# Kernel optimization log

Measured on AMD Instinct MI355X. Metric: run time of the kernel, lower is better.

The kernel has to match this reference:

```python
import jax, jax.numpy as jnp
import numpy as np

H = 56; W = 56; WS = 7; SHIFT = 3; C = 256; NH = 8
HD = C // NH; N = WS * WS; NW = (H // WS) * (W // WS)
SCALE = HD ** -0.5
LN_EPS = 1e-5


def _rel_pos_index():
    coords = np.stack(np.meshgrid(np.arange(WS), np.arange(WS), indexing='ij'))  # (2, ws, ws)
    cf = coords.reshape(2, -1)
    rel = (cf[:, :, None] - cf[:, None, :]).transpose(1, 2, 0)  # (N, N, 2)
    rel[..., 0] += WS - 1
    rel[..., 1] += WS - 1
    rel[..., 0] *= 2 * WS - 1
    return rel.sum(-1)  # (N, N) indices into (2*ws-1)^2 table

RPI = jnp.asarray(_rel_pos_index())


def _attn_mask():
    img = np.zeros((H, W))
    slices = (slice(0, -WS), slice(-WS, -SHIFT), slice(-SHIFT, None))
    cnt = 0
    for hs in slices:
        for ws_ in slices:
            img[hs, ws_] = cnt
            cnt += 1
    mw = img.reshape(H // WS, WS, W // WS, WS).transpose(0, 2, 1, 3).reshape(-1, N)
    diff = mw[:, None, :] - mw[:, :, None]  # (nW, N, N), [w,i,j] = mw[w,j]-mw[w,i]
    return jnp.asarray(np.where(diff != 0, -100.0, 0.0).astype(np.float32))

AMASK = _attn_mask()  # (nW, N, N)


def ln(x, g, b):
    m = x.mean(-1, keepdims=True)
    v = x.var(-1, keepdims=True)
    return (x - m) / jnp.sqrt(v + LN_EPS) * g + b


def win_part(x):  # (B, H, W, C) -> (B*nW, N, C)
    B = x.shape[0]
    return x.reshape(B, H // WS, WS, W // WS, WS, C).transpose(0, 1, 3, 2, 4, 5).reshape(-1, N, C)


def win_rev(xw, B):  # (B*nW, N, C) -> (B, H, W, C)
    return xw.reshape(B, H // WS, W // WS, WS, WS, C).transpose(0, 1, 3, 2, 4, 5).reshape(B, H, W, C)


def setup_inputs() -> dict:
    key = jax.random.key(0)
    ks = iter(jax.random.split(key, 40))
    B, L = 16, H * W
    Ch = int(C * 4.0)
    p = {}
    p['x'] = jax.random.normal(next(ks), (B, L, C), jnp.float32)
    p['x_SAR'] = jax.random.normal(next(ks), (B, L, C), jnp.float32)
    p['ln1_g'] = jnp.ones((C,)); p['ln1_b'] = jnp.zeros((C,))
    p['ln1s_g'] = jnp.ones((C,)); p['ln1s_b'] = jnp.zeros((C,))
    p['qkv_w'] = jax.random.normal(next(ks), (3 * C, C)) * 0.02
    p['qkv_b'] = jnp.zeros((3 * C,))
    p['qkvs_w'] = jax.random.normal(next(ks), (3 * C, C)) * 0.02
    p['qkvs_b'] = jnp.zeros((3 * C,))
    p['rpb_table'] = jax.random.normal(next(ks), ((2 * WS - 1) ** 2, NH)) * 0.02
    p['fuse_w'] = jax.random.normal(next(ks), (NH, NH)) * 0.1  # Conv2d(8,8,1) weight squeezed
    p['fuse_b'] = jnp.zeros((NH,))
    p['proj_w'] = jax.random.normal(next(ks), (C, C)) * 0.02
    p['proj_b'] = jnp.zeros((C,))
    p['projs_w'] = jax.random.normal(next(ks), (C, C)) * 0.02
    p['projs_b'] = jnp.zeros((C,))
    p['ln2_g'] = jnp.ones((C,)); p['ln2_b'] = jnp.zeros((C,))
    p['ln2s_g'] = jnp.ones((C,)); p['ln2s_b'] = jnp.zeros((C,))
    p['fc1_w'] = jax.random.normal(next(ks), (Ch, C)) * 0.02
    p['fc1_b'] = jnp.zeros((Ch,))
    p['fc2_w'] = jax.random.normal(next(ks), (C, Ch)) * 0.02
    p['fc2_b'] = jnp.zeros((C,))
    p['fc1s_w'] = jax.random.normal(next(ks), (Ch, C)) * 0.02
    p['fc1s_b'] = jnp.zeros((Ch,))
    p['fc2s_w'] = jax.random.normal(next(ks), (C, Ch)) * 0.02
    p['fc2s_b'] = jnp.zeros((C,))
    return p


def reference(x, x_SAR, ln1_g, ln1_b, ln1s_g, ln1s_b, qkv_w, qkv_b, qkvs_w, qkvs_b,
              rpb_table, fuse_w, fuse_b, proj_w, proj_b, projs_w, projs_b,
              ln2_g, ln2_b, ln2s_g, ln2s_b, fc1_w, fc1_b, fc2_w, fc2_b,
              fc1s_w, fc1s_b, fc2s_w, fc2s_b):
    B = x.shape[0]
    sc, sc_s = x, x_SAR

    def pre(xx, g, b):  # norm -> spatial -> cyclic shift -> windows
        xs = ln(xx, g, b).reshape(B, H, W, C)
        xs = jnp.roll(xs, (-SHIFT, -SHIFT), axis=(1, 2))
        return win_part(xs)

    xw = pre(x, ln1_g, ln1_b)
    xws = pre(x_SAR, ln1s_g, ln1s_b)

    def qkv_f(xin, Wt, bt):
        qkv = (xin @ Wt.T + bt).reshape(-1, N, 3, NH, HD).transpose(2, 0, 3, 1, 4)
        return qkv[0], qkv[1], qkv[2]  # each (B*nW, nH, N, HD)

    q, k, v = qkv_f(xw, qkv_w, qkv_b)
    qs, ks_, vs = qkv_f(xws, qkvs_w, qkvs_b)

    attn = jnp.einsum('bhnd,bhmd->bhnm', q * SCALE, k)
    attn_s = jnp.einsum('bhnd,bhmd->bhnm', qs * SCALE, ks_)

    rpb = rpb_table[RPI.reshape(-1)].reshape(N, N, NH).transpose(2, 0, 1)  # (nH, N, N)
    attn = attn + rpb[None]
    attn_s = attn_s + rpb[None]

    # shift-window mask add
    attn = (attn.reshape(B, NW, NH, N, N) + AMASK[None, :, None]).reshape(-1, NH, N, N)
    attn_s = (attn_s.reshape(B, NW, NH, N, N) + AMASK[None, :, None]).reshape(-1, NH, N, N)

    # dual-branch fusion: 1x1 conv over head dim + sigmoid gate
    diff = attn_s - attn
    gate = jax.nn.sigmoid(jnp.einsum('oh,bhnm->bonm', fuse_w, diff) + fuse_b[None, :, None, None])
    attn_f = jax.nn.softmax(attn + diff * gate, axis=-1)
    attn_s = jax.nn.softmax(attn_s, axis=-1)

    def out_f(a, vv, pw, pb):
        o = jnp.einsum('bhnm,bhmd->bhnd', a, vv).transpose(0, 2, 1, 3).reshape(-1, N, C)
        return o @ pw.T + pb

    xo = out_f(attn_f, v, proj_w, proj_b)
    xos = out_f(attn_s, vs, projs_w, projs_b)

    def post(xout, scc, g2, b2, w1, b1, w2, b2m):
        xr = jnp.roll(win_rev(xout, B), (SHIFT, SHIFT), axis=(1, 2)).reshape(B, -1, C)
        xr = scc + xr
        h = jax.nn.gelu(ln(xr, g2, b2) @ w1.T + b1, approximate=False)
        return xr + (h @ w2.T + b2m)

    out = post(xo, sc, ln2_g, ln2_b, fc1_w, fc1_b, fc2_w, fc2_b)
    out_s = post(xos, sc_s, ln2s_g, ln2s_b, fc1s_w, fc1s_b, fc2s_w, fc2s_b)
    return out, out_s
```

## Files before the change

### kernel.cpp

```cpp
#include <hip/hip_runtime.h>
#include <hip/hip_bf16.h>
#include <cstdio>

typedef unsigned short ushort_t;
using bf16x8  = __attribute__((ext_vector_type(8))) __bf16;
using u16x8   = __attribute__((ext_vector_type(8))) unsigned short;
using floatx4 = __attribute__((ext_vector_type(4))) float;

constexpr int    kTokens = 50176;
constexpr size_t TCsz    = (size_t)kTokens * 256;
constexpr float  kScale  = 0.17677669529663687f;
constexpr int    SPITCH  = 56;
constexpr size_t VTP     = 2048;
constexpr size_t VTSZ    = (size_t)8192 * VTP;

__device__ __forceinline__ float bf2f(ushort_t u) {
  unsigned int x = (unsigned int)u << 16;
  return __uint_as_float(x);
}
__device__ __forceinline__ ushort_t f2bf(float f) {
  __hip_bfloat16 h = __float2bfloat16(f);
  return *(ushort_t*)&h;
}

__device__ __forceinline__ void gl_lds16(const ushort_t* g, ushort_t* l) {
  __builtin_amdgcn_global_load_lds(
      (const __attribute__((address_space(1))) unsigned int*)g,
      (__attribute__((address_space(3))) unsigned int*)l, 16, 0, 0);
}

__global__ __launch_bounds__(256) void f2b_k(const float* __restrict__ src,
                                             ushort_t* __restrict__ dst, int n) {
  int i = blockIdx.x * 256 + threadIdx.x;
  if (i < n) dst[i] = f2bf(src[i]);
}

__global__ __launch_bounds__(64) void bias2_k(const float* __restrict__ rpb,
                                              float* __restrict__ biasf) {
  const int b = blockIdx.x;
  const int head = b & 7, chunk = (b >> 3) & 3, cls = b >> 5;
  const int wh7 = cls >> 1, ww7 = cls & 1;
  const int lane = threadIdx.x;
  float* bp = biasf + ((size_t)b * 64 + lane) * 16;
#pragma unroll
  for (int nt = 0; nt < 4; ++nt) {
#pragma unroll
    for (int r = 0; r < 4; ++r) {
      const int row = chunk * 16 + (lane >> 4) * 4 + r;
      const int col = nt * 16 + (lane & 15);
      float val = 0.0f;
      if (row < 49 && col < 49) {
        const int yi = row / 7, xi = row % 7, yj = col / 7, xj = col % 7;
        val = rpb[((yi - yj + 6) * 13 + (xi - xj + 6)) * 8 + head];
        const int li = (wh7 ? (yi < 4 ? 1 : 2) : 0) * 3 + (ww7 ? (xi < 4 ? 1 : 2) : 0);
        const int lj = (wh7 ? (yj < 4 ? 1 : 2) : 0) * 3 + (ww7 ? (xj < 4 ? 1 : 2) : 0);
        if (li != lj) val -= 100.0f;
      }
      bp[nt * 4 + r] = val;
    }
  }
}

__global__ __launch_bounds__(256) void vtz_k(ushort_t* __restrict__ vtA,
                                             ushort_t* __restrict__ vtB) {
  const int id = blockIdx.x * 256 + threadIdx.x;
  ushort_t* base = (id < 262144) ? vtA : vtB;
  const size_t r = (size_t)(id & 262143) * 64;
  const uint4 z{0, 0, 0, 0};
  *(uint4*)(base + r + 48) = z;
  *(uint4*)(base + r + 56) = z;
}

template <int SHIFTED>
__global__ __launch_bounds__(256) void ln_k(const float* __restrict__ x,
                                            const float* __restrict__ g,
                                            const float* __restrict__ b,
                                            ushort_t* __restrict__ yout) {
  const int wave = threadIdx.x >> 6, lane = threadIdx.x & 63;
  const int t = blockIdx.x * 4 + wave;
  size_t src;
  if (SHIFTED) {
    int bb = t / 3136, r = t % 3136;
    int wi = r / 49, n = r % 49;
    int hp = (wi >> 3) * 7 + n / 7;
    int wp = (wi & 7) * 7 + n % 7;
    int sh = hp + 3; if (sh >= 56) sh -= 56;
    int sw = wp + 3; if (sw >= 56) sw -= 56;
    src = ((size_t)bb * 3136 + sh * 56 + sw) * 256;
  } else {
    src = (size_t)t * 256;
  }
  const float4 v4 = *(const float4*)(x + src + lane * 4);
  float s  = v4.x + v4.y + v4.z + v4.w;
  float s2 = v4.x * v4.x + v4.y * v4.y + v4.z * v4.z + v4.w * v4.w;
#pragma unroll
  for (int off = 32; off > 0; off >>= 1) {
    s  += __shfl_xor(s,  off);
    s2 += __shfl_xor(s2, off);
  }
  const float mean = s * (1.0f / 256.0f);
  const float var  = s2 * (1.0f / 256.0f) - mean * mean;
  const float rstd = rsqrtf(var + 1e-5f);
  const float4 g4 = *(const float4*)(g + lane * 4);
  const float4 b4 = *(const float4*)(b + lane * 4);
  ushort4 o;
  o.x = f2bf((v4.x - mean) * rstd * g4.x + b4.x);
  o.y = f2bf((v4.y - mean) * rstd * g4.y + b4.y);
  o.z = f2bf((v4.z - mean) * rstd * g4.z + b4.z);
  o.w = f2bf((v4.w - mean) * rstd * g4.w + b4.w);
  *(ushort4*)(yout + (size_t)t * 256 + lane * 4) = o;
}

template <int MODE>
__global__ __launch_bounds__(256) void bgemm_k(const ushort_t* __restrict__ A,
                                               const ushort_t* __restrict__ W,
                                               const float* __restrict__ bias,
                                               float* __restrict__ outf,
                                               ushort_t* __restrict__ outb,
                                               const float* __restrict__ aux,
                                               int K, int Nc) {
  __shared__ __align__(16) ushort_t As[128 * 32];
  __shared__ __align__(16) ushort_t Bs[128 * 32];
  const int tid = threadIdx.x;
  const int nbx = gridDim.x;
  const int nwg = nbx * gridDim.y;
  int flat = blockIdx.y * nbx + blockIdx.x;
  {
    const int xcd = flat & 7, idx = flat >> 3;
    const int q8 = nwg >> 3, r8 = nwg & 7;
    flat = (xcd < r8 ? xcd * (q8 + 1) : r8 * (q8 + 1) + (xcd - r8) * q8) + idx;
  }
  const int m0 = (flat / nbx) * 128;
  const int n0 = (flat % nbx) * 128;
  const int lane = tid & 63, wv = tid >> 6;
  const int wm = (wv >> 1) * 64, wn = (wv & 1) * 64;
  const int l16 = lane & 15, quad = lane >> 4;

  const int srow = tid >> 2;
  const int gkc  = (tid & 3) ^ ((tid >> 3) & 3);
  const ushort_t* Ag0 = A + (size_t)(m0 + srow) * K + gkc * 8;
  const ushort_t* Ag1 = A + (size_t)(m0 + 64 + srow) * K + gkc * 8;
  const ushort_t* Wg0 = W + (size_t)(n0 + srow) * K + gkc * 8;
  const ushort_t* Wg1 = W + (size_t)(n0 + 64 + srow) * K + gkc * 8;
  ushort_t* AsW0 = As + wv * 512;
  ushort_t* AsW1 = As + 2048 + wv * 512;
  ushort_t* BsW0 = Bs + wv * 512;
  ushort_t* BsW1 = Bs + 2048 + wv * 512;

  const int kcq = quad ^ ((l16 >> 1) & 3);
  const int arA = (wm + l16) * 32 + kcq * 8;
  const int arB = (wn + l16) * 32 + kcq * 8;

  floatx4 acc[4][4] = {};
  for (int k0 = 0; k0 < K; k0 += 32) {
    gl_lds16(Ag0, AsW0);
    gl_lds16(Ag1, AsW1);
    gl_lds16(Wg0, BsW0);
    gl_lds16(Wg1, BsW1);
    Ag0 += 32; Ag1 += 32; Wg0 += 32; Wg1 += 32;
    __syncthreads();
    bf16x8 af[4], bfr[4];
#pragma unroll
    for (int t = 0; t < 4; ++t) {
      af[t]  = *(const bf16x8*)&As[arA + t * 512];
      bfr[t] = *(const bf16x8*)&Bs[arB + t * 512];
    }
#pragma unroll
    for (int mt = 0; mt < 4; ++mt)
#pragma unroll
      for (int nt = 0; nt < 4; ++nt)
        acc[mt][nt] = __builtin_amdgcn_mfma_f32_16x16x32_bf16(af[mt], bfr[nt], acc[mt][nt], 0, 0, 0);
    __syncthreads();
  }

  if (MODE == 0) {
    int wis[16], ns[16];
#pragma unroll
    for (int mt = 0; mt < 4; ++mt) {
      int row = m0 + wm + mt * 16 + quad * 4;
      int wi = row / 49, n = row - wi * 49;
#pragma unroll
      for (int r = 0; r < 4; ++r) {
        wis[mt * 4 + r] = wi; ns[mt * 4 + r] = n;
        if (++n == 49) { n = 0; ++wi; }
      }
    }
    if (n0 < 512) {
      size_t rb[16];
#pragma unroll
      for (int i = 0; i < 16; ++i) rb[i] = (size_t)wis[i] * 12544 + (size_t)ns[i] * 32;
#pragma unroll
      for (int nt = 0; nt < 4; ++nt) {
        const int col = n0 + wn + nt * 16 + l16;
        const int which = col >> 8, head = (col >> 5) & 7, d = col & 31;
        const float bv = bias[col];
        const float sc = (which == 0) ? kScale : 1.0f;
        ushort_t* ob = outb + (size_t)which * TCsz + head * 1568 + d;
#pragma unroll
        for (int i = 0; i < 16; ++i)
          ob[rb[i]] = f2bf((acc[i >> 2][nt][i & 3] + bv) * sc);
      }
    } else {
      size_t rb[16];
#pragma unroll
      for (int i = 0; i < 16; ++i) rb[i] = (size_t)wis[i] * 16384 + (size_t)ns[i];
      ushort_t* vtb = (ushort_t*)outf;
#pragma unroll
      for (int nt = 0; nt < 4; ++nt) {
        const int col = n0 + wn + nt * 16 + l16;
        const int head = (col >> 5) & 7, d = col & 31;
        const float bv = bias[col];
        ushort_t* ob = vtb + head * 2048 + d * 64;
#pragma unroll
        for (int i = 0; i < 16; ++i)
          ob[rb[i]] = f2bf(acc[i >> 2][nt][i & 3] + bv);
      }
    }
  } else if (MODE == 1) {
    size_t rb[16];
#pragma unroll
    for (int mt = 0; mt < 4; ++mt) {
#pragma unroll
      for (int r = 0; r < 4; ++r) {
        const int row = m0 + wm + mt * 16 + quad * 4 + r;
        const int wi = row / 49, n = row - wi * 49;
        const int b = wi >> 6, wl = wi & 63;
        int h = (wl >> 3) * 7 + n / 7 + 3; if (h >= 56) h -= 56;
        int w = (wl & 7) * 7 + n % 7 + 3; if (w >= 56) w -= 56;
        rb[mt * 4 + r] = ((size_t)(b * 3136 + h * 56 + w)) * 256;
      }
    }
#pragma unroll
    for (int nt = 0; nt < 4; ++nt) {
      const int col = n0 + wn + nt * 16 + l16;
      const float bv = bias[col];
#pragma unroll
      for (int i = 0; i < 16; ++i) {
        const size_t idx = rb[i] + col;
        outf[idx] = aux[idx] + acc[i >> 2][nt][i & 3] + bv;
      }
    }
  } else if (MODE == 2) {
    size_t rb[16];
#pragma unroll
    for (int mt = 0; mt < 4; ++mt)
#pragma unroll
      for (int r = 0; r < 4; ++r)
        rb[mt * 4 + r] = (size_t)(m0 + wm + mt * 16 + quad * 4 + r) * Nc;
#pragma unroll
    for (int nt = 0; nt < 4; ++nt) {
      const int col = n0 + wn + nt * 16 + l16;
      const float bv = bias[col];
#pragma unroll
      for (int i = 0; i < 16; ++i) {
        float val = acc[i >> 2][nt][i & 3] + bv;
        val = 0.5f * val * (1.0f + erff(val * 0.70710678118654752f));
        outb[rb[i] + col] = f2bf(val);
      }
    }
  } else {
    size_t rb[16];
#pragma unroll
    for (int mt = 0; mt < 4; ++mt)
#pragma unroll
      for (int r = 0; r < 4; ++r)
        rb[mt * 4 + r] = (size_t)(m0 + wm + mt * 16 + quad * 4 + r) * 256;
#pragma unroll
    for (int nt = 0; nt < 4; ++nt) {
      const int col = n0 + wn + nt * 16 + l16;
      const float bv = bias[col];
#pragma unroll
      for (int i = 0; i < 16; ++i) {
        const size_t idx = rb[i] + col;
        outf[idx] = aux[idx] + acc[i >> 2][nt][i & 3] + bv;
      }
    }
  }
}

__global__ __launch_bounds__(256) void attn_k(const ushort_t* __restrict__ qA,
                                              const ushort_t* __restrict__ qB,
                                              const ushort_t* __restrict__ vtA,
                                              const ushort_t* __restrict__ vtB,
                                              const float* __restrict__ biasf,
                                              const float* __restrict__ fw,
                                              const float* __restrict__ fb,
                                              ushort_t* __restrict__ Obase) {
  __shared__ __align__(16) ushort_t S[16 * 16 * 56 + 64];
  __shared__ float fwl[64], fbl[8];
  __shared__ float linv[256];
  const int tid = threadIdx.x, lane = tid & 63, wv = tid >> 6;
  const int l16 = lane & 15, quad = lane >> 4;
  int bx = blockIdx.x;
  bx = (bx & 7) * 512 + (bx >> 3);
  const int win = bx >> 2, chunk = bx & 3;
  const int r0 = chunk * 16;
  const int rows = (r0 + 16 <= 49) ? 16 : (49 - r0);

  if (rows < 16) {
    const int per = (16 - rows) * 7;
    for (int u = tid; u < 16 * per; u += 256) {
      const int pr = u / per, off = u - pr * per;
      *(uint4*)(S + pr * 896 + rows * 56 + off * 8) = uint4{0, 0, 0, 0};
    }
  }
  if (tid < 16) *(uint4*)(S + 14336 + tid * 8) = uint4{0, 0, 0, 0};
  if (tid < 64) fwl[tid] = fw[tid];
  if (tid < 8)  fbl[tid] = fb[tid];
  __syncthreads();

  const int wl = win & 63;
  const int cls = (((wl >> 3) == 7) ? 2 : 0) + (((wl & 7) == 7) ? 1 : 0);

  const int qrow = (r0 + l16 <= 48) ? (r0 + l16) : 48;
  for (int i = 0; i < 4; ++i) {
    const int pair = wv * 4 + i;
    const int br = pair >> 3, h = pair & 7;
    const ushort_t* qb = (br ? qB : qA) + (size_t)(win * 8 + h) * 1568;
    const ushort_t* kb = qb + TCsz;
    const bf16x8 af = *(const bf16x8*)(qb + qrow * 32 + quad * 8);
    floatx4 acc[4];
#pragma unroll
    for (int nt = 0; nt < 4; ++nt) {
      const int krow = nt * 16 + l16;
      const int krc = (krow <= 48) ? krow : 48;
      const bf16x8 bfr = *(const bf16x8*)(kb + krc * 32 + quad * 8);
      acc[nt] = __builtin_amdgcn_mfma_f32_16x16x32_bf16(af, bfr, (floatx4){0.f, 0.f, 0.f, 0.f}, 0, 0, 0);
    }
    const float* bfp = biasf + ((size_t)((cls * 4 + chunk) * 8 + h) * 64 + lane) * 16;
    ushort_t* Sp = S + pair * 896;
#pragma unroll
    for (int nt = 0; nt < 4; ++nt) {
      const int col = nt * 16 + l16;
      if (col >= SPITCH) continue;
      const float4 bv4 = *(const float4*)(bfp + nt * 4);
      const float bvv[4] = {bv4.x, bv4.y, bv4.z, bv4.w};
#pragma unroll
      for (int r = 0; r < 4; ++r) {
        const int lrow = quad * 4 + r;
        if (lrow < rows)
          Sp[lrow * 56 + col] = (col < 49) ? f2bf(acc[nt][r] + bvv[r]) : (ushort_t)0;
      }
    }
  }
  __syncthreads();

  const int np = rows * 49;
  for (int p = tid; p < np; p += 256) {
    const int lr = p / 49, c = p - lr * 49;
    const int off = lr * 56 + c;
    float sA[8], dd[8];
#pragma unroll
    for (int h = 0; h < 8; ++h) {
      sA[h] = bf2f(S[h * 896 + off]);
      dd[h] = bf2f(S[(8 + h) * 896 + off]) - sA[h];
    }
#pragma unroll
    for (int o = 0; o < 8; ++o) {
      float g = fbl[o];
#pragma unroll
      for (int h = 0; h < 8; ++h) g = fmaf(fwl[o * 8 + h], dd[h], g);
      g = __builtin_amdgcn_rcpf(1.0f + __expf(-g));
      S[o * 896 + off] = f2bf(sA[o] + dd[o] * g);
    }
  }
  __syncthreads();

  {
    const int lr = tid & 15, ph = tid >> 4;
    if (lr < rows) {
      ushort_t* row = S + ph * 896 + lr * 56;
      bf16x8 c[7];
#pragma unroll
      for (int j = 0; j < 7; ++j) c[j] = *(const bf16x8*)(row + j * 8);
      float mx = -1e30f;
#pragma unroll
      for (int j = 0; j < 6; ++j)
#pragma unroll
        for (int e = 0; e < 8; ++e) mx = fmaxf(mx, (float)c[j][e]);
      mx = fmaxf(mx, (float)c[6][0]);
      float sum = 0.0f;
#pragma unroll
      for (int j = 0; j < 6; ++j) {
        u16x8 o;
#pragma unroll
        for (int e = 0; e < 8; ++e) {
          const float ev = __expf((float)c[j][e] - mx);
          sum += ev;
          o[e] = f2bf(ev);
        }
        *(u16x8*)(row + j * 8) = o;
      }
      {
        const float ev = __expf((float)c[6][0] - mx);
        sum += ev;
        u16x8 o = {};
        o[0] = f2bf(ev);
        *(u16x8*)(row + 48) = o;
      }
      linv[tid] = __builtin_amdgcn_rcpf(sum);
    } else {
      linv[tid] = 1.0f;
    }
  }
  __syncthreads();

  for (int i = 0; i < 4; ++i) {
    const int pair = wv * 4 + i;
    const int br = pair >> 3, h = pair & 7;
    const ushort_t* vt = (br ? vtB : vtA) + (size_t)(win * 8 + h) * VTP;
    const ushort_t* Sp = S + pair * 896;
    floatx4 acc[2] = {};
#pragma unroll
    for (int ks = 0; ks < 2; ++ks) {
      const bf16x8 af = *(const bf16x8*)(Sp + l16 * 56 + ks * 32 + quad * 8);
#pragma unroll
      for (int nt = 0; nt < 2; ++nt) {
        const bf16x8 bv = *(const bf16x8*)(vt + (nt * 16 + l16) * 64 + ks * 32 + quad * 8);
        acc[nt] = __builtin_amdgcn_mfma_f32_16x16x32_bf16(af, bv, acc[nt], 0, 0, 0);
      }
    }
    ushort_t* Ob = Obase + (size_t)br * TCsz + (size_t)(win * 49 + r0) * 256 + h * 32;
#pragma unroll
    for (int nt = 0; nt < 2; ++nt)
#pragma unroll
      for (int r = 0; r < 4; ++r) {
        const int n = quad * 4 + r;
        if (n < rows)
          Ob[(size_t)n * 256 + nt * 16 + l16] = f2bf(acc[nt][r] * linv[pair * 16 + n]);
      }
  }
}

extern "C" void kernel_launch(void* const* d_in, const int* in_sizes, int n_in,
                              void* d_out, int out_size, void* d_ws, size_t ws_size,
                              hipStream_t stream) {
  if (n_in < 29) { fprintf(stderr, "kernel_launch: expected 29 inputs, got %d\n", n_in); return; }
  const float* x      = (const float*)d_in[0];
  const float* xsar   = (const float*)d_in[1];
  const float* ln1_g  = (const float*)d_in[2];
  const float* ln1_b  = (const float*)d_in[3];
  const float* ln1s_g = (const float*)d_in[4];
  const float* ln1s_b = (const float*)d_in[5];
  const float* qkv_w  = (const float*)d_in[6];
  const float* qkv_b  = (const float*)d_in[7];
  const float* qkvs_w = (const float*)d_in[8];
  const float* qkvs_b = (const float*)d_in[9];
  const float* rpb    = (const float*)d_in[10];
  const float* fuse_w = (const float*)d_in[11];
  const float* fuse_b = (const float*)d_in[12];
  const float* proj_w = (const float*)d_in[13];
  const float* proj_b = (const float*)d_in[14];
  const float* projs_w = (const float*)d_in[15];
  const float* projs_b = (const float*)d_in[16];
  const float* ln2_g  = (const float*)d_in[17];
  const float* ln2_b  = (const float*)d_in[18];
  const float* ln2s_g = (const float*)d_in[19];
  const float* ln2s_b = (const float*)d_in[20];
  const float* fc1_w  = (const float*)d_in[21];
  const float* fc1_b  = (const float*)d_in[22];
  const float* fc2_w  = (const float*)d_in[23];
  const float* fc2_b  = (const float*)d_in[24];
  const float* fc1s_w = (const float*)d_in[25];
  const float* fc1s_b = (const float*)d_in[26];
  const float* fc2s_w = (const float*)d_in[27];
  const float* fc2s_b = (const float*)d_in[28];
  float* out = (float*)d_out;
  float* ws  = (float*)d_ws;

  const size_t need = 8 * TCsz * sizeof(float);
  if (ws_size < need) {
    fprintf(stderr, "kernel_launch: ws_size %zu < needed %zu\n", ws_size, need);
    return;
  }

  ushort_t* H   = (ushort_t*)ws;
  ushort_t* xw  = H;
  ushort_t* xws = H + TCsz;
  ushort_t* q   = H + 2 * TCsz;
  ushort_t* qs  = H + 5 * TCsz;
  ushort_t* vtA = H + 8 * TCsz;
  ushort_t* vtB = vtA + VTSZ;
  float* xr  = ws + 6 * TCsz;
  float* xrs = ws + 7 * TCsz;
  ushort_t* y   = H + 2 * TCsz;
  ushort_t* ysb = H + 3 * TCsz;
  ushort_t* hbuf = H + 4 * TCsz;
  ushort_t* wb  = H + 12 * TCsz - 1572864;
  float* biasf = (float*)(H + 12 * TCsz - 1572864 - 262144);
  ushort_t* wqkv  = wb;
  ushort_t* wqkvs = wb + 196608;
  ushort_t* wproj = wb + 393216;
  ushort_t* wprojs= wb + 458752;
  ushort_t* wfc1  = wb + 524288;
  ushort_t* wfc1s = wb + 786432;
  ushort_t* wfc2  = wb + 1048576;
  ushort_t* wfc2s = wb + 1310720;

  f2b_k<<<768, 256, 0, stream>>>(qkv_w,  wqkv,  196608);
  f2b_k<<<768, 256, 0, stream>>>(qkvs_w, wqkvs, 196608);
  f2b_k<<<256, 256, 0, stream>>>(proj_w, wproj, 65536);
  f2b_k<<<256, 256, 0, stream>>>(projs_w,wprojs,65536);
  f2b_k<<<1024,256, 0, stream>>>(fc1_w,  wfc1,  262144);
  f2b_k<<<1024,256, 0, stream>>>(fc1s_w, wfc1s, 262144);
  f2b_k<<<1024,256, 0, stream>>>(fc2_w,  wfc2,  262144);
  f2b_k<<<1024,256, 0, stream>>>(fc2s_w, wfc2s, 262144);
  bias2_k<<<128, 64, 0, stream>>>(rpb, biasf);
  vtz_k<<<2048, 256, 0, stream>>>(vtA, vtB);

  ln_k<1><<<12544, 256, 0, stream>>>(x,    ln1_g,  ln1_b,  xw);
  ln_k<1><<<12544, 256, 0, stream>>>(xsar, ln1s_g, ln1s_b, xws);
  bgemm_k<0><<<dim3(6, 392), 256, 0, stream>>>(xw,  wqkv,  qkv_b,  (float*)vtA, q,  nullptr, 256, 768);
  bgemm_k<0><<<dim3(6, 392), 256, 0, stream>>>(xws, wqkvs, qkvs_b, (float*)vtB, qs, nullptr, 256, 768);
  attn_k<<<4096, 256, 0, stream>>>(q, qs, vtA, vtB, biasf, fuse_w, fuse_b, H);
  bgemm_k<1><<<dim3(2, 392), 256, 0, stream>>>(H,        wproj,  proj_b,  xr,  nullptr, x,    256, 256);
  bgemm_k<1><<<dim3(2, 392), 256, 0, stream>>>(H + TCsz, wprojs, projs_b, xrs, nullptr, xsar, 256, 256);
  ln_k<0><<<12544, 256, 0, stream>>>(xr,  ln2_g,  ln2_b,  y);
  ln_k<0><<<12544, 256, 0, stream>>>(xrs, ln2s_g, ln2s_b, ysb);
  bgemm_k<2><<<dim3(8, 392), 256, 0, stream>>>(y,    wfc1,  fc1_b,  nullptr, hbuf, nullptr, 256, 1024);
  bgemm_k<3><<<dim3(2, 392), 256, 0, stream>>>(hbuf, wfc2,  fc2_b,  out,     nullptr, xr,  1024, 256);
  bgemm_k<2><<<dim3(8, 392), 256, 0, stream>>>(ysb,  wfc1s, fc1s_b, nullptr, hbuf, nullptr, 256, 1024);
  bgemm_k<3><<<dim3(2, 392), 256, 0, stream>>>(hbuf, wfc2s, fc2s_b, out + TCsz, nullptr, xrs, 1024, 256);
}
```

Before: 937.9 us.

## Double-buffer GEMM LDS tiles and pad attention score plane stride

The bf16 GEMM now double-buffers its A/B LDS tiles, issuing global-to-LDS loads for the next K step before the MFMAs on the current one, and needs only one barrier per iteration. In the attention kernel each head's score plane gets a padded stride of 904 instead of 896 to spread LDS bank usage, and the QK and PV head loops are unrolled. This doubles GEMM LDS use, which may reduce occupancy, and the padding slightly enlarges the attention scratch.

```diff
diff --git a/kernel.cpp b/kernel.cpp
--- a/kernel.cpp
+++ b/kernel.cpp
@@ -10,7 +10,7 @@
 constexpr int    kTokens = 50176;
 constexpr size_t TCsz    = (size_t)kTokens * 256;
 constexpr float  kScale  = 0.17677669529663687f;
-constexpr int    SPITCH  = 56;
+constexpr int    PSTR    = 904;
 constexpr size_t VTP     = 2048;
 constexpr size_t VTSZ    = (size_t)8192 * VTP;
 
@@ -119,8 +119,8 @@
                                                ushort_t* __restrict__ outb,
                                                const float* __restrict__ aux,
                                                int K, int Nc) {
-  __shared__ __align__(16) ushort_t As[128 * 32];
-  __shared__ __align__(16) ushort_t Bs[128 * 32];
+  __shared__ __align__(16) ushort_t As[2 * 4096];
+  __shared__ __align__(16) ushort_t Bs[2 * 4096];
   const int tid = threadIdx.x;
   const int nbx = gridDim.x;
   const int nwg = nbx * gridDim.y;
@@ -142,28 +142,37 @@
   const ushort_t* Ag1 = A + (size_t)(m0 + 64 + srow) * K + gkc * 8;
   const ushort_t* Wg0 = W + (size_t)(n0 + srow) * K + gkc * 8;
   const ushort_t* Wg1 = W + (size_t)(n0 + 64 + srow) * K + gkc * 8;
-  ushort_t* AsW0 = As + wv * 512;
-  ushort_t* AsW1 = As + 2048 + wv * 512;
-  ushort_t* BsW0 = Bs + wv * 512;
-  ushort_t* BsW1 = Bs + 2048 + wv * 512;
+  const int ldsW0 = wv * 512, ldsW1 = 2048 + wv * 512;
 
   const int kcq = quad ^ ((l16 >> 1) & 3);
   const int arA = (wm + l16) * 32 + kcq * 8;
   const int arB = (wn + l16) * 32 + kcq * 8;
 
+  const int NT = K >> 5;
   floatx4 acc[4][4] = {};
-  for (int k0 = 0; k0 < K; k0 += 32) {
-    gl_lds16(Ag0, AsW0);
-    gl_lds16(Ag1, AsW1);
-    gl_lds16(Wg0, BsW0);
-    gl_lds16(Wg1, BsW1);
-    Ag0 += 32; Ag1 += 32; Wg0 += 32; Wg1 += 32;
-    __syncthreads();
+
+  gl_lds16(Ag0, As + ldsW0);
+  gl_lds16(Ag1, As + ldsW1);
+  gl_lds16(Wg0, Bs + ldsW0);
+  gl_lds16(Wg1, Bs + ldsW1);
+  __syncthreads();
+
+  int cur = 0;
+  for (int t = 0; t < NT; ++t) {
+    if (t + 1 < NT) {
+      const int k0 = (t + 1) * 32;
+      const int nb = (cur ^ 1) * 4096;
+      gl_lds16(Ag0 + k0, As + nb + ldsW0);
+      gl_lds16(Ag1 + k0, As + nb + ldsW1);
+      gl_lds16(Wg0 + k0, Bs + nb + ldsW0);
+      gl_lds16(Wg1 + k0, Bs + nb + ldsW1);
+    }
+    const int cb = cur * 4096;
     bf16x8 af[4], bfr[4];
 #pragma unroll
-    for (int t = 0; t < 4; ++t) {
-      af[t]  = *(const bf16x8*)&As[arA + t * 512];
-      bfr[t] = *(const bf16x8*)&Bs[arB + t * 512];
+    for (int tt = 0; tt < 4; ++tt) {
+      af[tt]  = *(const bf16x8*)&As[cb + arA + tt * 512];
+      bfr[tt] = *(const bf16x8*)&Bs[cb + arB + tt * 512];
     }
 #pragma unroll
     for (int mt = 0; mt < 4; ++mt)
@@ -171,6 +180,7 @@
       for (int nt = 0; nt < 4; ++nt)
         acc[mt][nt] = __builtin_amdgcn_mfma_f32_16x16x32_bf16(af[mt], bfr[nt], acc[mt][nt], 0, 0, 0);
     __syncthreads();
+    cur ^= 1;
   }
 
   if (MODE == 0) {
@@ -286,7 +296,7 @@
                                               const float* __restrict__ fw,
                                               const float* __restrict__ fb,
                                               ushort_t* __restrict__ Obase) {
-  __shared__ __align__(16) ushort_t S[16 * 16 * 56 + 64];
+  __shared__ __align__(16) ushort_t S[16 * PSTR];
   __shared__ float fwl[64], fbl[8];
   __shared__ float linv[256];
   const int tid = threadIdx.x, lane = tid & 63, wv = tid >> 6;
@@ -301,10 +311,10 @@
     const int per = (16 - rows) * 7;
     for (int u = tid; u < 16 * per; u += 256) {
       const int pr = u / per, off = u - pr * per;
-      *(uint4*)(S + pr * 896 + rows * 56 + off * 8) = uint4{0, 0, 0, 0};
-    }
-  }
-  if (tid < 16) *(uint4*)(S + 14336 + tid * 8) = uint4{0, 0, 0, 0};
+      *(uint4*)(S + pr * PSTR + rows * 56 + off * 8) = uint4{0, 0, 0, 0};
+    }
+  }
+  if (tid < 16) *(uint4*)(S + tid * PSTR + 896) = uint4{0, 0, 0, 0};
   if (tid < 64) fwl[tid] = fw[tid];
   if (tid < 8)  fbl[tid] = fb[tid];
   __syncthreads();
@@ -313,6 +323,7 @@
   const int cls = (((wl >> 3) == 7) ? 2 : 0) + (((wl & 7) == 7) ? 1 : 0);
 
   const int qrow = (r0 + l16 <= 48) ? (r0 + l16) : 48;
+#pragma unroll
   for (int i = 0; i < 4; ++i) {
     const int pair = wv * 4 + i;
     const int br = pair >> 3, h = pair & 7;
@@ -328,11 +339,11 @@
       acc[nt] = __builtin_amdgcn_mfma_f32_16x16x32_bf16(af, bfr, (floatx4){0.f, 0.f, 0.f, 0.f}, 0, 0, 0);
     }
     const float* bfp = biasf + ((size_t)((cls * 4 + chunk) * 8 + h) * 64 + lane) * 16;
-    ushort_t* Sp = S + pair * 896;
+    ushort_t* Sp = S + pair * PSTR;
 #pragma unroll
     for (int nt = 0; nt < 4; ++nt) {
       const int col = nt * 16 + l16;
-      if (col >= SPITCH) continue;
+      if (col >= 56) continue;
       const float4 bv4 = *(const float4*)(bfp + nt * 4);
       const float bvv[4] = {bv4.x, bv4.y, bv4.z, bv4.w};
 #pragma unroll
@@ -352,8 +363,8 @@
     float sA[8], dd[8];
 #pragma unroll
     for (int h = 0; h < 8; ++h) {
-      sA[h] = bf2f(S[h * 896 + off]);
-      dd[h] = bf2f(S[(8 + h) * 896 + off]) - sA[h];
+      sA[h] = bf2f(S[h * PSTR + off]);
+      dd[h] = bf2f(S[(8 + h) * PSTR + off]) - sA[h];
     }
 #pragma unroll
     for (int o = 0; o < 8; ++o) {
@@ -361,7 +372,7 @@
 #pragma unroll
       for (int h = 0; h < 8; ++h) g = fmaf(fwl[o * 8 + h], dd[h], g);
       g = __builtin_amdgcn_rcpf(1.0f + __expf(-g));
-      S[o * 896 + off] = f2bf(sA[o] + dd[o] * g);
+      S[o * PSTR + off] = f2bf(sA[o] + dd[o] * g);
     }
   }
   __syncthreads();
@@ -369,7 +380,7 @@
   {
     const int lr = tid & 15, ph = tid >> 4;
     if (lr < rows) {
-      ushort_t* row = S + ph * 896 + lr * 56;
+      ushort_t* row = S + ph * PSTR + lr * 56;
       bf16x8 c[7];
 #pragma unroll
       for (int j = 0; j < 7; ++j) c[j] = *(const bf16x8*)(row + j * 8);
@@ -405,11 +416,12 @@
   }
   __syncthreads();
 
+#pragma unroll
   for (int i = 0; i < 4; ++i) {
     const int pair = wv * 4 + i;
     const int br = pair >> 3, h = pair & 7;
     const ushort_t* vt = (br ? vtB : vtA) + (size_t)(win * 8 + h) * VTP;
-    const ushort_t* Sp = S + pair * 896;
+    const ushort_t* Sp = S + pair * PSTR;
     floatx4 acc[2] = {};
 #pragma unroll
     for (int ks = 0; ks < 2; ++ks) {
```

New measurement: 928.8 us. Within noise of the previous version (-1.0%).
